# Kernel optimization log

Measured on AMD Instinct MI355X. Metric: run time of the kernel, lower is better.

## Reference

```python
import jax, jax.numpy as jnp
import numpy as np

B, N, D, H, K, T = 32, 4096, 256, 4, 8, 3
D_H = D // H
SCALE = D_H ** -0.5
EPS = 1e-8
LN_EPS = 1e-5


def _ln(x, g, b):
    m = x.mean(-1, keepdims=True)
    v = ((x - m) ** 2).mean(-1, keepdims=True)
    return (x - m) / jnp.sqrt(v + LN_EPS) * g + b


def _split(t):  # [b, n, D] -> [b, H, n, d_h]
    b, n, _ = t.shape
    return t.reshape(b, n, H, D_H).transpose(0, 2, 1, 3)


def _merge(t):  # [b, H, n, d_h] -> [b, n, D]
    b, h, n, d = t.shape
    return t.transpose(0, 2, 1, 3).reshape(b, n, h * d)


def setup_inputs() -> dict:
    key = jax.random.key(0)
    ks = jax.random.split(key, 12)
    init = lambda k, shape: (jax.random.normal(k, shape, jnp.float32) * 0.02)
    mu = jnp.tile(jnp.linspace(-1.0, 1.0, K)[:, None], (1, D))[None]  # [1,K,D]
    return {
        'x': jax.random.normal(ks[0], (B, N, D), jnp.float32),
        'mu': mu,
        'w_q': init(ks[1], (D, D)),
        'w_k': init(ks[2], (D, D)),
        'w_v': init(ks[3], (D, D)),
        'w_comb': init(ks[4], (D, D)),
        'g_in': jnp.ones(D), 'b_in': jnp.zeros(D),
        'g_slot': jnp.ones(D), 'b_slot': jnp.zeros(D),
        'g_mlp': jnp.ones(D), 'b_mlp': jnp.zeros(D),
        'w_ih': init(ks[5], (3 * D, D)),
        'w_hh': init(ks[6], (3 * D, D)),
        'b_ih': jnp.zeros(3 * D),
        'b_hh': jnp.zeros(3 * D),
        'w1': init(ks[7], (D, D)), 'b1': jnp.zeros(D),
        'w2': init(ks[8], (D, D)), 'b2': jnp.zeros(D),
    }


def reference(x, mu, w_q, w_k, w_v, w_comb, g_in, b_in, g_slot, b_slot,
              g_mlp, b_mlp, w_ih, w_hh, b_ih, b_hh, w1, b1, w2, b2):
    b = x.shape[0]
    x_norm = _ln(x, g_in, b_in)
    k_feat = _split(x_norm @ w_k.T)  # [b,H,N,d_h]
    v_feat = _split(x_norm @ w_v.T)

    def gru(u, h):  # torch GRUCell semantics
        gi = u @ w_ih.T + b_ih
        gh = h @ w_hh.T + b_hh
        ir, iz, i_n = jnp.split(gi, 3, axis=-1)
        hr, hz, h_n = jnp.split(gh, 3, axis=-1)
        r = jax.nn.sigmoid(ir + hr)
        z = jax.nn.sigmoid(iz + hz)
        n = jnp.tanh(i_n + r * h_n)
        return (1.0 - z) * n + z * h

    def step(slots, _):
        q = _split(_ln(slots, g_slot, b_slot) @ w_q.T)  # [b,H,K,d_h]
        dots = jnp.einsum('bhkd,bhnd->bhkn', q, k_feat) * SCALE
        attn = jax.nn.softmax(dots, axis=-2)  # softmax over slots
        attn = attn / (attn.sum(axis=-1, keepdims=True) + EPS)  # renorm over inputs
        updates = _merge(jnp.einsum('bhkn,bhnd->bhkd', attn, v_feat)) @ w_comb.T
        new = gru(updates.reshape(-1, D), slots.reshape(-1, D)).reshape(slots.shape)
        hid = jnp.maximum(_ln(new, g_mlp, b_mlp) @ w1.T + b1, 0.0)
        new = new + (hid @ w2.T + b2)
        return new, None

    slots0 = jnp.broadcast_to(mu, (b, K, D))  # eval mode: slots = mu
    slots, _ = jax.lax.scan(step, slots0, None, length=T)
    return slots
```

## Files before the change

kernel.cpp:

```cpp
#include <hip/hip_runtime.h>

#define BB 32
#define NN 4096
#define DD 256
#define HH 4
#define KK 8
#define DH 64

typedef unsigned short u16;
typedef unsigned int u32;
typedef __attribute__((ext_vector_type(8))) short short8;
typedef __attribute__((ext_vector_type(4))) float f32x4;

__device__ __forceinline__ float b2f(u16 u){ return __uint_as_float(((u32)u)<<16); }
__device__ __forceinline__ u16 f2b(float f){
  u32 u = __float_as_uint(f);
  u32 r = (u + 0x7fffu + ((u>>16)&1u)) >> 16;
  return (u16)r;
}

__global__ __launch_bounds__(256) void prep_kernel(
    const float* __restrict__ mu, const float* __restrict__ w_q,
    const float* __restrict__ w_k, const float* __restrict__ w_v,
    const float* __restrict__ w_comb, const float* __restrict__ w_ih,
    const float* __restrict__ w_hh, const float* __restrict__ w1,
    const float* __restrict__ w2,
    u16* __restrict__ wkv, u16* __restrict__ wq_b, u16* __restrict__ wcomb_b,
    u16* __restrict__ wih_b, u16* __restrict__ whh_b, u16* __restrict__ w1_b,
    u16* __restrict__ w2_b, float* __restrict__ slots)
{
  int i = blockIdx.x*256 + threadIdx.x;
  if (i < 131072) {
    int c = i>>8, d = i&255;
    float v = (c<256) ? w_k[c*256+d] : w_v[(c-256)*256+d];
    int off = (c<<9) + ((2*d) ^ ((c&15)<<4));
    wkv[off>>1] = f2b(v);
    return;
  }
  i -= 131072;
  if (i < 65536){ wq_b[i] = f2b(w_q[i]); return; } i -= 65536;
  if (i < 65536){ wcomb_b[i] = f2b(w_comb[i]); return; } i -= 65536;
  if (i < 196608){ wih_b[i] = f2b(w_ih[i]); return; } i -= 196608;
  if (i < 196608){ whh_b[i] = f2b(w_hh[i]); return; } i -= 196608;
  if (i < 65536){ w1_b[i] = f2b(w1[i]); return; } i -= 65536;
  if (i < 65536){ w2_b[i] = f2b(w2[i]); return; } i -= 65536;
  if (i < 65536){ slots[i] = mu[i & 2047]; return; }
}

__global__ __launch_bounds__(512,4) void kv_proj_kernel(
    const float* __restrict__ x, const float* __restrict__ g_in,
    const float* __restrict__ b_in, const u16* __restrict__ wkv,
    u16* __restrict__ Kmat, u16* __restrict__ Vmat)
{
  __shared__ __align__(16) u16 Atile[64*256];
  __shared__ __align__(16) u16 Btile[64*256];
  __shared__ __align__(16) u16 Cbuf[64*64];
  const int tid = threadIdx.x;
  const int w = tid>>6, l = tid&63;
  const long row0 = (long)blockIdx.x * 64;

  short8 breg[4];
  #pragma unroll
  for (int i=0;i<4;++i)
    breg[i] = *(const short8*)((const char*)wkv + (i*512 + tid)*16);

  const f32x4 gv = *(const f32x4*)(g_in + l*4);
  const f32x4 bv = *(const f32x4*)(b_in + l*4);

  #pragma unroll
  for (int rr=0; rr<8; ++rr) {
    const int r = w*8 + rr;
    const f32x4 xv = *(const f32x4*)(x + (row0+r)*DD + l*4);
    float s = xv.x+xv.y+xv.z+xv.w;
    float s2 = xv.x*xv.x+xv.y*xv.y+xv.z*xv.z+xv.w*xv.w;
    #pragma unroll
    for (int m=1;m<64;m<<=1){ s += __shfl_xor(s,m); s2 += __shfl_xor(s2,m); }
    const float mean = s * (1.f/256.f);
    const float rstd = rsqrtf(s2*(1.f/256.f) - mean*mean + 1e-5f);
    const u32 p0 = (u32)f2b((xv.x-mean)*rstd*gv.x + bv.x) | ((u32)f2b((xv.y-mean)*rstd*gv.y + bv.y)<<16);
    const u32 p1 = (u32)f2b((xv.z-mean)*rstd*gv.z + bv.z) | ((u32)f2b((xv.w-mean)*rstd*gv.w + bv.w)<<16);
    const unsigned long long pp = (unsigned long long)p0 | ((unsigned long long)p1<<32);
    *(unsigned long long*)((char*)Atile + r*512 + ((l*8) ^ ((r&15)<<4))) = pp;
  }
  #pragma unroll
  for (int i=0;i<4;++i)
    *(short8*)((char*)Btile + (i*512+tid)*16) = breg[i];
  __syncthreads();

  const int wm = w>>2, wn = w&3;
  const int lr = l&15;
  const int lk = (l>>4)*8;

  short8 afr0[8], afr1[8];
  #pragma unroll
  for (int ks=0; ks<8; ++ks) {
    const int k2 = (ks*32 + lk)*2;
    const int r0r = wm*32 + lr;
    const int r1r = wm*32 + 16 + lr;
    afr0[ks] = *(const short8*)((const char*)Atile + r0r*512 + (k2 ^ ((r0r&15)<<4)));
    afr1[ks] = *(const short8*)((const char*)Atile + r1r*512 + (k2 ^ ((r1r&15)<<4)));
  }
  #pragma unroll
  for (int ks=0; ks<8; ++ks) {
    asm volatile("" : "+v"(afr0[ks]));
    asm volatile("" : "+v"(afr1[ks]));
  }

  for (int ct=0; ct<8; ++ct) {
    short8 nreg[4];
    if (ct < 7) {
      #pragma unroll
      for (int i=0;i<4;++i)
        nreg[i] = *(const short8*)((const char*)wkv + (ct+1)*32768 + (i*512 + tid)*16);
    }

    f32x4 acc0 = (f32x4)0.f, acc1 = (f32x4)0.f;
    #pragma unroll
    for (int ks=0; ks<8; ++ks) {
      const int k2 = (ks*32 + lk)*2;
      const int c = wn*16 + lr;
      const short8 bfv = *(const short8*)((const char*)Btile + c*512 + (k2 ^ ((c&15)<<4)));
      acc0 = __builtin_amdgcn_mfma_f32_16x16x32_bf16(afr0[ks], bfv, acc0, 0,0,0);
      acc1 = __builtin_amdgcn_mfma_f32_16x16x32_bf16(afr1[ks], bfv, acc1, 0,0,0);
    }

    {
      const int c = wn*16 + lr;
      #pragma unroll
      for (int reg=0; reg<4; ++reg) {
        const int r0r = wm*32 + (l>>4)*4 + reg;
        const int r1r = r0r + 16;
        *(u16*)((char*)Cbuf + r0r*128 + ((2*c) ^ ((r0r&7)<<4))) = f2b(acc0[reg]);
        *(u16*)((char*)Cbuf + r1r*128 + ((2*c) ^ ((r1r&7)<<4))) = f2b(acc1[reg]);
      }
    }
    __syncthreads();

    if (ct < 7) {
      #pragma unroll
      for (int i=0;i<4;++i)
        *(short8*)((char*)Btile + (i*512+tid)*16) = nreg[i];
    }
    {
      const int r = tid>>3, cg = tid&7;
      const short8 vv = *(const short8*)((char*)Cbuf + r*128 + ((cg*16) ^ ((r&7)<<4)));
      u16* dst = (ct<4) ? Kmat : Vmat;
      *(short8*)(dst + (row0+r)*DD + (ct&3)*64 + cg*8) = vv;
    }
    __syncthreads();
  }
}

__global__ __launch_bounds__(256) void slot_q_kernel(
    const float* __restrict__ slots, const float* __restrict__ g_slot,
    const float* __restrict__ b_slot, const u16* __restrict__ wq_b,
    float* __restrict__ qmat)
{
  __shared__ float xn[256];
  __shared__ float red[8];
  const int r = blockIdx.x, t = threadIdx.x;
  const int w = t>>6, l = t&63;
  const float xv = slots[r*256 + t];
  float s = xv, s2 = xv*xv;
  #pragma unroll
  for (int m=1;m<64;m<<=1){ s += __shfl_xor(s,m); s2 += __shfl_xor(s2,m); }
  if (l==0){ red[w*2]=s; red[w*2+1]=s2; }
  __syncthreads();
  s = red[0]+red[2]+red[4]+red[6];
  s2 = red[1]+red[3]+red[5]+red[7];
  const float mean = s*(1.f/256.f);
  const float rstd = rsqrtf(s2*(1.f/256.f)-mean*mean + 1e-5f);
  xn[t] = (xv-mean)*rstd*g_slot[t] + b_slot[t];
  __syncthreads();
  const u16* wr = wq_b + t*256;
  float a0=0,a1=0,a2=0,a3=0;
  for (int d=0; d<256; d+=8) {
    const short8 wv = *(const short8*)(wr + d);
    a0 = fmaf(b2f((u16)wv[0]), xn[d+0], a0);
    a1 = fmaf(b2f((u16)wv[1]), xn[d+1], a1);
    a2 = fmaf(b2f((u16)wv[2]), xn[d+2], a2);
    a3 = fmaf(b2f((u16)wv[3]), xn[d+3], a3);
    a0 = fmaf(b2f((u16)wv[4]), xn[d+4], a0);
    a1 = fmaf(b2f((u16)wv[5]), xn[d+5], a1);
    a2 = fmaf(b2f((u16)wv[6]), xn[d+6], a2);
    a3 = fmaf(b2f((u16)wv[7]), xn[d+7], a3);
  }
  qmat[r*256 + t] = ((a0+a1)+(a2+a3));
}

__global__ __launch_bounds__(256) void attn_kernel(
    const u16* __restrict__ Kmat, const u16* __restrict__ Vmat,
    const float* __restrict__ qmat, float* __restrict__ U_part,
    float* __restrict__ S_part)
{
  __shared__ float U_lds[4][8][64];
  __shared__ float S_lds[4][8];
  const int bid = blockIdx.x;
  const int part = bid & 3, h = (bid>>2)&3, b = bid>>4;
  const int t = threadIdx.x, w = t>>6, l = t&63;
  const int ds = l&7, ng = l>>3;

  float qreg[8][8];
  #pragma unroll
  for (int k=0;k<8;++k) {
    const f32x4 qa = *(const f32x4*)(qmat + (b*8+k)*256 + h*64 + ds*8);
    const f32x4 qb = *(const f32x4*)(qmat + (b*8+k)*256 + h*64 + ds*8 + 4);
    qreg[k][0]=qa.x; qreg[k][1]=qa.y; qreg[k][2]=qa.z; qreg[k][3]=qa.w;
    qreg[k][4]=qb.x; qreg[k][5]=qb.y; qreg[k][6]=qb.z; qreg[k][7]=qb.w;
  }

  float accU[8][8];
  float sacc[8];
  #pragma unroll
  for (int k=0;k<8;++k){ sacc[k]=0.f;
    #pragma unroll
    for (int j=0;j<8;++j) accU[k][j]=0.f; }

  const long base = ((long)b*NN)*DD + h*64;
  const u16* Kp = Kmat + base + (long)(part*1024 + w*8 + ng)*DD + ds*8;
  const u16* Vp = Vmat + base + (long)(part*1024 + w*8 + ng)*DD + ds*8;

  short8 kc = *(const short8*)Kp;
  short8 vc = *(const short8*)Vp;
  for (int pass=0; pass<32; ++pass) {
    short8 kn, vn;
    if (pass < 31) {
      kn = *(const short8*)(Kp + (pass+1)*32*DD);
      vn = *(const short8*)(Vp + (pass+1)*32*DD);
    }
    float kd[8];
    #pragma unroll
    for (int j=0;j<8;++j) kd[j] = b2f((u16)kc[j]);
    float dots[8];
    #pragma unroll
    for (int k=0;k<8;++k) {
      float d0 = qreg[k][0]*kd[0] + qreg[k][1]*kd[1] + qreg[k][2]*kd[2] + qreg[k][3]*kd[3]
               + qreg[k][4]*kd[4] + qreg[k][5]*kd[5] + qreg[k][6]*kd[6] + qreg[k][7]*kd[7];
      d0 += __shfl_xor(d0,1); d0 += __shfl_xor(d0,2); d0 += __shfl_xor(d0,4);
      dots[k] = d0 * 0.125f;
    }
    float mx = dots[0];
    #pragma unroll
    for (int k=1;k<8;++k) mx = fmaxf(mx, dots[k]);
    float e[8]; float se = 0.f;
    #pragma unroll
    for (int k=0;k<8;++k){ e[k] = __expf(dots[k]-mx); se += e[k]; }
    const float inv = 1.f/se;
    float vd[8];
    #pragma unroll
    for (int j=0;j<8;++j) vd[j] = b2f((u16)vc[j]);
    #pragma unroll
    for (int k=0;k<8;++k) {
      const float p = e[k]*inv;
      sacc[k] += p;
      #pragma unroll
      for (int j=0;j<8;++j) accU[k][j] = fmaf(p, vd[j], accU[k][j]);
    }
    kc = kn; vc = vn;
  }
  #pragma unroll
  for (int k=0;k<8;++k){
    #pragma unroll
    for (int j=0;j<8;++j){
      float v = accU[k][j];
      v += __shfl_xor(v,8); v += __shfl_xor(v,16); v += __shfl_xor(v,32);
      accU[k][j]=v;
    }
    float sv = sacc[k];
    sv += __shfl_xor(sv,8); sv += __shfl_xor(sv,16); sv += __shfl_xor(sv,32);
    sacc[k]=sv;
  }
  if (l<8){
    #pragma unroll
    for (int k=0;k<8;++k)
      #pragma unroll
      for (int j=0;j<8;++j) U_lds[w][k][l*8+j] = accU[k][j];
  }
  if (l==0){
    #pragma unroll
    for (int k=0;k<8;++k) S_lds[w][k]=sacc[k];
  }
  __syncthreads();
  for (int i=t;i<512;i+=256){
    const int k=i>>6, d=i&63;
    U_part[(((long)part*32 + b)*4 + h)*512 + k*64 + d] =
      U_lds[0][k][d]+U_lds[1][k][d]+U_lds[2][k][d]+U_lds[3][k][d];
  }
  if (t<8){
    S_part[((part*32 + b)*4 + h)*8 + t] = S_lds[0][t]+S_lds[1][t]+S_lds[2][t]+S_lds[3][t];
  }
}

__global__ __launch_bounds__(256) void slot_update_kernel(
    const float* __restrict__ U_part, const float* __restrict__ S_part,
    float* __restrict__ slots,
    const u16* __restrict__ wcomb_b, const u16* __restrict__ wih_b,
    const u16* __restrict__ whh_b, const u16* __restrict__ w1_b,
    const u16* __restrict__ w2_b,
    const float* __restrict__ b_ih, const float* __restrict__ b_hh,
    const float* __restrict__ g_mlp, const float* __restrict__ b_mlp,
    const float* __restrict__ b1v, const float* __restrict__ b2v,
    const u16* __restrict__ wq_b, const float* __restrict__ g_slot,
    const float* __restrict__ b_slot, float* __restrict__ qmat,
    float* __restrict__ out_final, const int write_out, const int compute_q)
{
  __shared__ float uL[2][256];
  __shared__ float hL[2][256];
  __shared__ float cL[2][256];
  __shared__ float xL[2][256];
  __shared__ float red[16];
  const int blk = blockIdx.x, t = threadIdx.x;
  const int w = t>>6, l = t&63;
  const int r0 = blk*2;

  #pragma unroll
  for (int rr=0;rr<2;++rr) hL[rr][t] = slots[(r0+rr)*256 + t];

  #pragma unroll
  for (int rr=0;rr<2;++rr) {
    const int r = r0+rr, b = r>>3, k = r&7;
    const int h = t>>6, d = t&63;
    float ssum = 0.f, usum = 0.f;
    #pragma unroll
    for (int p=0;p<4;++p) {
      ssum += S_part[((p*32 + b)*4 + h)*8 + k];
      usum += U_part[(((long)p*32 + b)*4 + h)*512 + k*64 + d];
    }
    uL[rr][t] = usum / (ssum + 1e-8f);
  }
  __syncthreads();

  {
    float c00=0,c01=0,c10=0,c11=0;
    const u16* wr = wcomb_b + t*256;
    for (int d0=0; d0<256; d0+=8) {
      const short8 wv = *(const short8*)(wr + d0);
      float wf[8];
      #pragma unroll
      for (int j=0;j<8;++j) wf[j]=b2f((u16)wv[j]);
      #pragma unroll
      for (int j=0;j<8;j+=2) {
        c00 = fmaf(wf[j],   uL[0][d0+j],   c00);
        c01 = fmaf(wf[j+1], uL[0][d0+j+1], c01);
        c10 = fmaf(wf[j],   uL[1][d0+j],   c10);
        c11 = fmaf(wf[j+1], uL[1][d0+j+1], c11);
      }
    }
    cL[0][t]=c00+c01; cL[1][t]=c10+c11;
  }
  __syncthreads();

  float gi[3][2], gh[3][2];
  #pragma unroll
  for (int g=0; g<3; ++g){ gi[g][0]=0; gi[g][1]=0; gh[g][0]=0; gh[g][1]=0; }
  for (int d0=0; d0<256; d0+=8) {
    float u0[8],u1[8],h0[8],h1[8];
    #pragma unroll
    for (int j=0;j<8;j+=4) {
      *(f32x4*)&u0[j] = *(const f32x4*)&cL[0][d0+j];
      *(f32x4*)&u1[j] = *(const f32x4*)&cL[1][d0+j];
      *(f32x4*)&h0[j] = *(const f32x4*)&hL[0][d0+j];
      *(f32x4*)&h1[j] = *(const f32x4*)&hL[1][d0+j];
    }
    #pragma unroll
    for (int g=0; g<3; ++g) {
      const short8 wi = *(const short8*)(wih_b + (g*256+t)*256 + d0);
      const short8 wh = *(const short8*)(whh_b + (g*256+t)*256 + d0);
      #pragma unroll
      for (int j=0;j<8;++j) {
        const float a = b2f((u16)wi[j]);
        const float bw = b2f((u16)wh[j]);
        gi[g][0] = fmaf(a, u0[j], gi[g][0]);
        gi[g][1] = fmaf(a, u1[j], gi[g][1]);
        gh[g][0] = fmaf(bw, h0[j], gh[g][0]);
        gh[g][1] = fmaf(bw, h1[j], gh[g][1]);
      }
    }
  }
  float newv[2];
  #pragma unroll
  for (int rr=0;rr<2;++rr) {
    const float ir = gi[0][rr] + b_ih[t];
    const float iz = gi[1][rr] + b_ih[256+t];
    const float inn= gi[2][rr] + b_ih[512+t];
    const float hr = gh[0][rr] + b_hh[t];
    const float hz = gh[1][rr] + b_hh[256+t];
    const float hn = gh[2][rr] + b_hh[512+t];
    const float rg = 1.f/(1.f + __expf(-(ir+hr)));
    const float zg = 1.f/(1.f + __expf(-(iz+hz)));
    float targ = inn + rg*hn;
    targ = fminf(fmaxf(targ, -15.f), 15.f);
    const float ex = __expf(2.f*targ);
    const float ng = (ex-1.f)/(ex+1.f);
    newv[rr] = (1.f-zg)*ng + zg*hL[rr][t];
  }

  float s0=newv[0], q0=newv[0]*newv[0], s1=newv[1], q1=newv[1]*newv[1];
  #pragma unroll
  for (int m=1;m<64;m<<=1){
    s0+=__shfl_xor(s0,m); q0+=__shfl_xor(q0,m);
    s1+=__shfl_xor(s1,m); q1+=__shfl_xor(q1,m);
  }
  if (l==0){ red[w*4]=s0; red[w*4+1]=q0; red[w*4+2]=s1; red[w*4+3]=q1; }
  __syncthreads();
  s0 = red[0]+red[4]+red[8]+red[12];
  q0 = red[1]+red[5]+red[9]+red[13];
  s1 = red[2]+red[6]+red[10]+red[14];
  q1 = red[3]+red[7]+red[11]+red[15];
  {
    const float m0 = s0*(1.f/256.f), m1 = s1*(1.f/256.f);
    const float r0v = rsqrtf(q0*(1.f/256.f)-m0*m0 + 1e-5f);
    const float r1v = rsqrtf(q1*(1.f/256.f)-m1*m1 + 1e-5f);
    xL[0][t] = (newv[0]-m0)*r0v*g_mlp[t] + b_mlp[t];
    xL[1][t] = (newv[1]-m1)*r1v*g_mlp[t] + b_mlp[t];
  }
  __syncthreads();

  {
    float c00=0,c01=0,c10=0,c11=0;
    const u16* wr = w1_b + t*256;
    for (int d0=0; d0<256; d0+=8) {
      const short8 wv = *(const short8*)(wr + d0);
      float wf[8];
      #pragma unroll
      for (int j=0;j<8;++j) wf[j]=b2f((u16)wv[j]);
      #pragma unroll
      for (int j=0;j<8;j+=2) {
        c00 = fmaf(wf[j],   xL[0][d0+j],   c00);
        c01 = fmaf(wf[j+1], xL[0][d0+j+1], c01);
        c10 = fmaf(wf[j],   xL[1][d0+j],   c10);
        c11 = fmaf(wf[j+1], xL[1][d0+j+1], c11);
      }
    }
    uL[0][t] = fmaxf(c00+c01 + b1v[t], 0.f);
    uL[1][t] = fmaxf(c10+c11 + b1v[t], 0.f);
  }
  __syncthreads();

  float o0, o1;
  {
    float c00=0,c01=0,c10=0,c11=0;
    const u16* wr = w2_b + t*256;
    for (int d0=0; d0<256; d0+=8) {
      const short8 wv = *(const short8*)(wr + d0);
      float wf[8];
      #pragma unroll
      for (int j=0;j<8;++j) wf[j]=b2f((u16)wv[j]);
      #pragma unroll
      for (int j=0;j<8;j+=2) {
        c00 = fmaf(wf[j],   uL[0][d0+j],   c00);
        c01 = fmaf(wf[j+1], uL[0][d0+j+1], c01);
        c10 = fmaf(wf[j],   uL[1][d0+j],   c10);
        c11 = fmaf(wf[j+1], uL[1][d0+j+1], c11);
      }
    }
    o0 = newv[0] + c00+c01 + b2v[t];
    o1 = newv[1] + c10+c11 + b2v[t];
    slots[(r0+0)*256 + t] = o0;
    slots[(r0+1)*256 + t] = o1;
    if (write_out){
      out_final[(r0+0)*256 + t] = o0;
      out_final[(r0+1)*256 + t] = o1;
    }
  }

  if (compute_q) {
    __syncthreads();
    float t0=o0, p0=o0*o0, t1=o1, p1=o1*o1;
    #pragma unroll
    for (int m=1;m<64;m<<=1){
      t0+=__shfl_xor(t0,m); p0+=__shfl_xor(p0,m);
      t1+=__shfl_xor(t1,m); p1+=__shfl_xor(p1,m);
    }
    if (l==0){ red[w*4]=t0; red[w*4+1]=p0; red[w*4+2]=t1; red[w*4+3]=p1; }
    __syncthreads();
    t0 = red[0]+red[4]+red[8]+red[12];
    p0 = red[1]+red[5]+red[9]+red[13];
    t1 = red[2]+red[6]+red[10]+red[14];
    p1 = red[3]+red[7]+red[11]+red[15];
    const float m0 = t0*(1.f/256.f), m1 = t1*(1.f/256.f);
    const float r0v = rsqrtf(p0*(1.f/256.f)-m0*m0 + 1e-5f);
    const float r1v = rsqrtf(p1*(1.f/256.f)-m1*m1 + 1e-5f);
    cL[0][t] = (o0-m0)*r0v*g_slot[t] + b_slot[t];
    cL[1][t] = (o1-m1)*r1v*g_slot[t] + b_slot[t];
    __syncthreads();
    float c00=0,c01=0,c10=0,c11=0;
    const u16* wr = wq_b + t*256;
    for (int d0=0; d0<256; d0+=8) {
      const short8 wv = *(const short8*)(wr + d0);
      float wf[8];
      #pragma unroll
      for (int j=0;j<8;++j) wf[j]=b2f((u16)wv[j]);
      #pragma unroll
      for (int j=0;j<8;j+=2) {
        c00 = fmaf(wf[j],   cL[0][d0+j],   c00);
        c01 = fmaf(wf[j+1], cL[0][d0+j+1], c01);
        c10 = fmaf(wf[j],   cL[1][d0+j],   c10);
        c11 = fmaf(wf[j+1], cL[1][d0+j+1], c11);
      }
    }
    qmat[(r0+0)*256 + t] = c00+c01;
    qmat[(r0+1)*256 + t] = c10+c11;
  }
}

extern "C" void kernel_launch(void* const* d_in, const int* in_sizes, int n_in,
                              void* d_out, int out_size, void* d_ws, size_t ws_size,
                              hipStream_t stream)
{
  (void)in_sizes; (void)n_in; (void)out_size; (void)ws_size;
  const float* x      = (const float*)d_in[0];
  const float* mu     = (const float*)d_in[1];
  const float* w_q    = (const float*)d_in[2];
  const float* w_k    = (const float*)d_in[3];
  const float* w_v    = (const float*)d_in[4];
  const float* w_comb = (const float*)d_in[5];
  const float* g_in   = (const float*)d_in[6];
  const float* b_in   = (const float*)d_in[7];
  const float* g_slot = (const float*)d_in[8];
  const float* b_slot = (const float*)d_in[9];
  const float* g_mlp  = (const float*)d_in[10];
  const float* b_mlp  = (const float*)d_in[11];
  const float* w_ih   = (const float*)d_in[12];
  const float* w_hh   = (const float*)d_in[13];
  const float* b_ih   = (const float*)d_in[14];
  const float* b_hh   = (const float*)d_in[15];
  const float* w1     = (const float*)d_in[16];
  const float* b1     = (const float*)d_in[17];
  const float* w2     = (const float*)d_in[18];
  const float* b2     = (const float*)d_in[19];

  char* ws = (char*)d_ws;
  u16* Kmat    = (u16*)(ws + 0);
  u16* Vmat    = (u16*)(ws + 67108864);
  u16* wkv     = (u16*)(ws + 134217728);
  u16* wq_b    = (u16*)(ws + 134479872);
  u16* wcomb_b = (u16*)(ws + 134610944);
  u16* wih_b   = (u16*)(ws + 134742016);
  u16* whh_b   = (u16*)(ws + 135135232);
  u16* w1_b    = (u16*)(ws + 135528448);
  u16* w2_b    = (u16*)(ws + 135659520);
  float* slots = (float*)(ws + 135790592);
  float* qmat  = (float*)(ws + 136052736);
  float* U_part= (float*)(ws + 136314880);
  float* S_part= (float*)(ws + 137363456);

  hipLaunchKernelGGL(prep_kernel, dim3(3328), dim3(256), 0, stream,
                     mu, w_q, w_k, w_v, w_comb, w_ih, w_hh, w1, w2,
                     wkv, wq_b, wcomb_b, wih_b, whh_b, w1_b, w2_b, slots);
  hipLaunchKernelGGL(kv_proj_kernel, dim3(2048), dim3(512), 0, stream,
                     x, g_in, b_in, wkv, Kmat, Vmat);
  hipLaunchKernelGGL(slot_q_kernel, dim3(256), dim3(256), 0, stream,
                     slots, g_slot, b_slot, wq_b, qmat);
  float* outp = (float*)d_out;
  for (int it=0; it<3; ++it) {
    hipLaunchKernelGGL(attn_kernel, dim3(512), dim3(256), 0, stream,
                       Kmat, Vmat, qmat, U_part, S_part);
    hipLaunchKernelGGL(slot_update_kernel, dim3(128), dim3(256), 0, stream,
                       U_part, S_part, slots, wcomb_b, wih_b, whh_b, w1_b, w2_b,
                       b_ih, b_hh, g_mlp, b_mlp, b1, b2,
                       wq_b, g_slot, b_slot, qmat,
                       outp, (it==2)?1:0, (it<2)?1:0);
  }
}
```

Before: 350.2 us.

## Fuse attention and slot-update iterations into one cooperative persistent kernel

Replaces six alternating attention and slot-update launches with a single cooperative kernel that loops over the three iterations and uses grid-wide syncs between phases. Blocks stride over the attention work units and the slot-update rows. The aim is to remove kernel launch and drain gaps between the short dependent stages. In exchange it adds grid.sync overhead and a launch_bounds occupancy hint of 2 blocks per CU, which may cost registers in the heavy attention loop. The grid size also depends on the occupancy query, and with 256 blocks each block would do two attention units.

```diff
diff --git a/kernel.cpp b/kernel.cpp
--- a/kernel.cpp
+++ b/kernel.cpp
@@ -1,4 +1,5 @@
 #include <hip/hip_runtime.h>
+#include <hip/hip_cooperative_groups.h>
 
 #define BB 32
 #define NN 4096
@@ -188,111 +189,9 @@
   qmat[r*256 + t] = ((a0+a1)+(a2+a3));
 }
 
-__global__ __launch_bounds__(256) void attn_kernel(
+__global__ __launch_bounds__(256,2) void mega_kernel(
     const u16* __restrict__ Kmat, const u16* __restrict__ Vmat,
-    const float* __restrict__ qmat, float* __restrict__ U_part,
-    float* __restrict__ S_part)
-{
-  __shared__ float U_lds[4][8][64];
-  __shared__ float S_lds[4][8];
-  const int bid = blockIdx.x;
-  const int part = bid & 3, h = (bid>>2)&3, b = bid>>4;
-  const int t = threadIdx.x, w = t>>6, l = t&63;
-  const int ds = l&7, ng = l>>3;
-
-  float qreg[8][8];
-  #pragma unroll
-  for (int k=0;k<8;++k) {
-    const f32x4 qa = *(const f32x4*)(qmat + (b*8+k)*256 + h*64 + ds*8);
-    const f32x4 qb = *(const f32x4*)(qmat + (b*8+k)*256 + h*64 + ds*8 + 4);
-    qreg[k][0]=qa.x; qreg[k][1]=qa.y; qreg[k][2]=qa.z; qreg[k][3]=qa.w;
-    qreg[k][4]=qb.x; qreg[k][5]=qb.y; qreg[k][6]=qb.z; qreg[k][7]=qb.w;
-  }
-
-  float accU[8][8];
-  float sacc[8];
-  #pragma unroll
-  for (int k=0;k<8;++k){ sacc[k]=0.f;
-    #pragma unroll
-    for (int j=0;j<8;++j) accU[k][j]=0.f; }
-
-  const long base = ((long)b*NN)*DD + h*64;
-  const u16* Kp = Kmat + base + (long)(part*1024 + w*8 + ng)*DD + ds*8;
-  const u16* Vp = Vmat + base + (long)(part*1024 + w*8 + ng)*DD + ds*8;
-
-  short8 kc = *(const short8*)Kp;
-  short8 vc = *(const short8*)Vp;
-  for (int pass=0; pass<32; ++pass) {
-    short8 kn, vn;
-    if (pass < 31) {
-      kn = *(const short8*)(Kp + (pass+1)*32*DD);
-      vn = *(const short8*)(Vp + (pass+1)*32*DD);
-    }
-    float kd[8];
-    #pragma unroll
-    for (int j=0;j<8;++j) kd[j] = b2f((u16)kc[j]);
-    float dots[8];
-    #pragma unroll
-    for (int k=0;k<8;++k) {
-      float d0 = qreg[k][0]*kd[0] + qreg[k][1]*kd[1] + qreg[k][2]*kd[2] + qreg[k][3]*kd[3]
-               + qreg[k][4]*kd[4] + qreg[k][5]*kd[5] + qreg[k][6]*kd[6] + qreg[k][7]*kd[7];
-      d0 += __shfl_xor(d0,1); d0 += __shfl_xor(d0,2); d0 += __shfl_xor(d0,4);
-      dots[k] = d0 * 0.125f;
-    }
-    float mx = dots[0];
-    #pragma unroll
-    for (int k=1;k<8;++k) mx = fmaxf(mx, dots[k]);
-    float e[8]; float se = 0.f;
-    #pragma unroll
-    for (int k=0;k<8;++k){ e[k] = __expf(dots[k]-mx); se += e[k]; }
-    const float inv = 1.f/se;
-    float vd[8];
-    #pragma unroll
-    for (int j=0;j<8;++j) vd[j] = b2f((u16)vc[j]);
-    #pragma unroll
-    for (int k=0;k<8;++k) {
-      const float p = e[k]*inv;
-      sacc[k] += p;
-      #pragma unroll
-      for (int j=0;j<8;++j) accU[k][j] = fmaf(p, vd[j], accU[k][j]);
-    }
-    kc = kn; vc = vn;
-  }
-  #pragma unroll
-  for (int k=0;k<8;++k){
-    #pragma unroll
-    for (int j=0;j<8;++j){
-      float v = accU[k][j];
-      v += __shfl_xor(v,8); v += __shfl_xor(v,16); v += __shfl_xor(v,32);
-      accU[k][j]=v;
-    }
-    float sv = sacc[k];
-    sv += __shfl_xor(sv,8); sv += __shfl_xor(sv,16); sv += __shfl_xor(sv,32);
-    sacc[k]=sv;
-  }
-  if (l<8){
-    #pragma unroll
-    for (int k=0;k<8;++k)
-      #pragma unroll
-      for (int j=0;j<8;++j) U_lds[w][k][l*8+j] = accU[k][j];
-  }
-  if (l==0){
-    #pragma unroll
-    for (int k=0;k<8;++k) S_lds[w][k]=sacc[k];
-  }
-  __syncthreads();
-  for (int i=t;i<512;i+=256){
-    const int k=i>>6, d=i&63;
-    U_part[(((long)part*32 + b)*4 + h)*512 + k*64 + d] =
-      U_lds[0][k][d]+U_lds[1][k][d]+U_lds[2][k][d]+U_lds[3][k][d];
-  }
-  if (t<8){
-    S_part[((part*32 + b)*4 + h)*8 + t] = S_lds[0][t]+S_lds[1][t]+S_lds[2][t]+S_lds[3][t];
-  }
-}
-
-__global__ __launch_bounds__(256) void slot_update_kernel(
-    const float* __restrict__ U_part, const float* __restrict__ S_part,
+    float* __restrict__ qmat, float* __restrict__ U_part, float* __restrict__ S_part,
     float* __restrict__ slots,
     const u16* __restrict__ wcomb_b, const u16* __restrict__ wih_b,
     const u16* __restrict__ whh_b, const u16* __restrict__ w1_b,
@@ -301,206 +200,317 @@
     const float* __restrict__ g_mlp, const float* __restrict__ b_mlp,
     const float* __restrict__ b1v, const float* __restrict__ b2v,
     const u16* __restrict__ wq_b, const float* __restrict__ g_slot,
-    const float* __restrict__ b_slot, float* __restrict__ qmat,
-    float* __restrict__ out_final, const int write_out, const int compute_q)
+    const float* __restrict__ b_slot, float* __restrict__ out_final)
 {
+  cooperative_groups::grid_group grid = cooperative_groups::this_grid();
+  __shared__ float U_lds[4][8][64];
+  __shared__ float S_lds[4][8];
   __shared__ float uL[2][256];
   __shared__ float hL[2][256];
   __shared__ float cL[2][256];
   __shared__ float xL[2][256];
   __shared__ float red[16];
-  const int blk = blockIdx.x, t = threadIdx.x;
-  const int w = t>>6, l = t&63;
-  const int r0 = blk*2;
-
-  #pragma unroll
-  for (int rr=0;rr<2;++rr) hL[rr][t] = slots[(r0+rr)*256 + t];
-
-  #pragma unroll
-  for (int rr=0;rr<2;++rr) {
-    const int r = r0+rr, b = r>>3, k = r&7;
-    const int h = t>>6, d = t&63;
-    float ssum = 0.f, usum = 0.f;
-    #pragma unroll
-    for (int p=0;p<4;++p) {
-      ssum += S_part[((p*32 + b)*4 + h)*8 + k];
-      usum += U_part[(((long)p*32 + b)*4 + h)*512 + k*64 + d];
-    }
-    uL[rr][t] = usum / (ssum + 1e-8f);
-  }
-  __syncthreads();
-
-  {
-    float c00=0,c01=0,c10=0,c11=0;
-    const u16* wr = wcomb_b + t*256;
-    for (int d0=0; d0<256; d0+=8) {
-      const short8 wv = *(const short8*)(wr + d0);
-      float wf[8];
-      #pragma unroll
-      for (int j=0;j<8;++j) wf[j]=b2f((u16)wv[j]);
-      #pragma unroll
-      for (int j=0;j<8;j+=2) {
-        c00 = fmaf(wf[j],   uL[0][d0+j],   c00);
-        c01 = fmaf(wf[j+1], uL[0][d0+j+1], c01);
-        c10 = fmaf(wf[j],   uL[1][d0+j],   c10);
-        c11 = fmaf(wf[j+1], uL[1][d0+j+1], c11);
-      }
-    }
-    cL[0][t]=c00+c01; cL[1][t]=c10+c11;
-  }
-  __syncthreads();
-
-  float gi[3][2], gh[3][2];
-  #pragma unroll
-  for (int g=0; g<3; ++g){ gi[g][0]=0; gi[g][1]=0; gh[g][0]=0; gh[g][1]=0; }
-  for (int d0=0; d0<256; d0+=8) {
-    float u0[8],u1[8],h0[8],h1[8];
-    #pragma unroll
-    for (int j=0;j<8;j+=4) {
-      *(f32x4*)&u0[j] = *(const f32x4*)&cL[0][d0+j];
-      *(f32x4*)&u1[j] = *(const f32x4*)&cL[1][d0+j];
-      *(f32x4*)&h0[j] = *(const f32x4*)&hL[0][d0+j];
-      *(f32x4*)&h1[j] = *(const f32x4*)&hL[1][d0+j];
-    }
-    #pragma unroll
-    for (int g=0; g<3; ++g) {
-      const short8 wi = *(const short8*)(wih_b + (g*256+t)*256 + d0);
-      const short8 wh = *(const short8*)(whh_b + (g*256+t)*256 + d0);
-      #pragma unroll
-      for (int j=0;j<8;++j) {
-        const float a = b2f((u16)wi[j]);
-        const float bw = b2f((u16)wh[j]);
-        gi[g][0] = fmaf(a, u0[j], gi[g][0]);
-        gi[g][1] = fmaf(a, u1[j], gi[g][1]);
-        gh[g][0] = fmaf(bw, h0[j], gh[g][0]);
-        gh[g][1] = fmaf(bw, h1[j], gh[g][1]);
-      }
-    }
-  }
-  float newv[2];
-  #pragma unroll
-  for (int rr=0;rr<2;++rr) {
-    const float ir = gi[0][rr] + b_ih[t];
-    const float iz = gi[1][rr] + b_ih[256+t];
-    const float inn= gi[2][rr] + b_ih[512+t];
-    const float hr = gh[0][rr] + b_hh[t];
-    const float hz = gh[1][rr] + b_hh[256+t];
-    const float hn = gh[2][rr] + b_hh[512+t];
-    const float rg = 1.f/(1.f + __expf(-(ir+hr)));
-    const float zg = 1.f/(1.f + __expf(-(iz+hz)));
-    float targ = inn + rg*hn;
-    targ = fminf(fmaxf(targ, -15.f), 15.f);
-    const float ex = __expf(2.f*targ);
-    const float ng = (ex-1.f)/(ex+1.f);
-    newv[rr] = (1.f-zg)*ng + zg*hL[rr][t];
-  }
-
-  float s0=newv[0], q0=newv[0]*newv[0], s1=newv[1], q1=newv[1]*newv[1];
-  #pragma unroll
-  for (int m=1;m<64;m<<=1){
-    s0+=__shfl_xor(s0,m); q0+=__shfl_xor(q0,m);
-    s1+=__shfl_xor(s1,m); q1+=__shfl_xor(q1,m);
-  }
-  if (l==0){ red[w*4]=s0; red[w*4+1]=q0; red[w*4+2]=s1; red[w*4+3]=q1; }
-  __syncthreads();
-  s0 = red[0]+red[4]+red[8]+red[12];
-  q0 = red[1]+red[5]+red[9]+red[13];
-  s1 = red[2]+red[6]+red[10]+red[14];
-  q1 = red[3]+red[7]+red[11]+red[15];
-  {
-    const float m0 = s0*(1.f/256.f), m1 = s1*(1.f/256.f);
-    const float r0v = rsqrtf(q0*(1.f/256.f)-m0*m0 + 1e-5f);
-    const float r1v = rsqrtf(q1*(1.f/256.f)-m1*m1 + 1e-5f);
-    xL[0][t] = (newv[0]-m0)*r0v*g_mlp[t] + b_mlp[t];
-    xL[1][t] = (newv[1]-m1)*r1v*g_mlp[t] + b_mlp[t];
-  }
-  __syncthreads();
-
-  {
-    float c00=0,c01=0,c10=0,c11=0;
-    const u16* wr = w1_b + t*256;
-    for (int d0=0; d0<256; d0+=8) {
-      const short8 wv = *(const short8*)(wr + d0);
-      float wf[8];
-      #pragma unroll
-      for (int j=0;j<8;++j) wf[j]=b2f((u16)wv[j]);
-      #pragma unroll
-      for (int j=0;j<8;j+=2) {
-        c00 = fmaf(wf[j],   xL[0][d0+j],   c00);
-        c01 = fmaf(wf[j+1], xL[0][d0+j+1], c01);
-        c10 = fmaf(wf[j],   xL[1][d0+j],   c10);
-        c11 = fmaf(wf[j+1], xL[1][d0+j+1], c11);
-      }
-    }
-    uL[0][t] = fmaxf(c00+c01 + b1v[t], 0.f);
-    uL[1][t] = fmaxf(c10+c11 + b1v[t], 0.f);
-  }
-  __syncthreads();
-
-  float o0, o1;
-  {
-    float c00=0,c01=0,c10=0,c11=0;
-    const u16* wr = w2_b + t*256;
-    for (int d0=0; d0<256; d0+=8) {
-      const short8 wv = *(const short8*)(wr + d0);
-      float wf[8];
-      #pragma unroll
-      for (int j=0;j<8;++j) wf[j]=b2f((u16)wv[j]);
-      #pragma unroll
-      for (int j=0;j<8;j+=2) {
-        c00 = fmaf(wf[j],   uL[0][d0+j],   c00);
-        c01 = fmaf(wf[j+1], uL[0][d0+j+1], c01);
-        c10 = fmaf(wf[j],   uL[1][d0+j],   c10);
-        c11 = fmaf(wf[j+1], uL[1][d0+j+1], c11);
-      }
-    }
-    o0 = newv[0] + c00+c01 + b2v[t];
-    o1 = newv[1] + c10+c11 + b2v[t];
-    slots[(r0+0)*256 + t] = o0;
-    slots[(r0+1)*256 + t] = o1;
-    if (write_out){
-      out_final[(r0+0)*256 + t] = o0;
-      out_final[(r0+1)*256 + t] = o1;
-    }
-  }
-
-  if (compute_q) {
-    __syncthreads();
-    float t0=o0, p0=o0*o0, t1=o1, p1=o1*o1;
-    #pragma unroll
-    for (int m=1;m<64;m<<=1){
-      t0+=__shfl_xor(t0,m); p0+=__shfl_xor(p0,m);
-      t1+=__shfl_xor(t1,m); p1+=__shfl_xor(p1,m);
-    }
-    if (l==0){ red[w*4]=t0; red[w*4+1]=p0; red[w*4+2]=t1; red[w*4+3]=p1; }
-    __syncthreads();
-    t0 = red[0]+red[4]+red[8]+red[12];
-    p0 = red[1]+red[5]+red[9]+red[13];
-    t1 = red[2]+red[6]+red[10]+red[14];
-    p1 = red[3]+red[7]+red[11]+red[15];
-    const float m0 = t0*(1.f/256.f), m1 = t1*(1.f/256.f);
-    const float r0v = rsqrtf(p0*(1.f/256.f)-m0*m0 + 1e-5f);
-    const float r1v = rsqrtf(p1*(1.f/256.f)-m1*m1 + 1e-5f);
-    cL[0][t] = (o0-m0)*r0v*g_slot[t] + b_slot[t];
-    cL[1][t] = (o1-m1)*r1v*g_slot[t] + b_slot[t];
-    __syncthreads();
-    float c00=0,c01=0,c10=0,c11=0;
-    const u16* wr = wq_b + t*256;
-    for (int d0=0; d0<256; d0+=8) {
-      const short8 wv = *(const short8*)(wr + d0);
-      float wf[8];
-      #pragma unroll
-      for (int j=0;j<8;++j) wf[j]=b2f((u16)wv[j]);
-      #pragma unroll
-      for (int j=0;j<8;j+=2) {
-        c00 = fmaf(wf[j],   cL[0][d0+j],   c00);
-        c01 = fmaf(wf[j+1], cL[0][d0+j+1], c01);
-        c10 = fmaf(wf[j],   cL[1][d0+j],   c10);
-        c11 = fmaf(wf[j+1], cL[1][d0+j+1], c11);
-      }
-    }
-    qmat[(r0+0)*256 + t] = c00+c01;
-    qmat[(r0+1)*256 + t] = c10+c11;
+
+  const int G = gridDim.x;
+  const int t = threadIdx.x, w = t>>6, l = t&63;
+
+  for (int it=0; it<3; ++it) {
+    for (int u = blockIdx.x; u < 512; u += G) {
+      const int part = u & 3, h = (u>>2)&3, b = u>>4;
+      const int ds = l&7, ng = l>>3;
+
+      float qreg[8][8];
+      #pragma unroll
+      for (int k=0;k<8;++k) {
+        const f32x4 qa = *(const f32x4*)(qmat + (b*8+k)*256 + h*64 + ds*8);
+        const f32x4 qb = *(const f32x4*)(qmat + (b*8+k)*256 + h*64 + ds*8 + 4);
+        qreg[k][0]=qa.x; qreg[k][1]=qa.y; qreg[k][2]=qa.z; qreg[k][3]=qa.w;
+        qreg[k][4]=qb.x; qreg[k][5]=qb.y; qreg[k][6]=qb.z; qreg[k][7]=qb.w;
+      }
+
+      float accU[8][8];
+      float sacc[8];
+      #pragma unroll
+      for (int k=0;k<8;++k){ sacc[k]=0.f;
+        #pragma unroll
+        for (int j=0;j<8;++j) accU[k][j]=0.f; }
+
+      const long base = ((long)b*NN)*DD + h*64;
+      const u16* Kp = Kmat + base + (long)(part*1024 + w*8 + ng)*DD + ds*8;
+      const u16* Vp = Vmat + base + (long)(part*1024 + w*8 + ng)*DD + ds*8;
+
+      short8 kc = *(const short8*)Kp;
+      short8 vc = *(const short8*)Vp;
+      for (int pass=0; pass<32; ++pass) {
+        short8 kn = kc, vn = vc;
+        if (pass < 31) {
+          kn = *(const short8*)(Kp + (pass+1)*32*DD);
+          vn = *(const short8*)(Vp + (pass+1)*32*DD);
+        }
+        float kd[8];
+        #pragma unroll
+        for (int j=0;j<8;++j) kd[j] = b2f((u16)kc[j]);
+        float dots[8];
+        #pragma unroll
+        for (int k=0;k<8;++k) {
+          float d0 = qreg[k][0]*kd[0] + qreg[k][1]*kd[1] + qreg[k][2]*kd[2] + qreg[k][3]*kd[3]
+                   + qreg[k][4]*kd[4] + qreg[k][5]*kd[5] + qreg[k][6]*kd[6] + qreg[k][7]*kd[7];
+          d0 += __shfl_xor(d0,1); d0 += __shfl_xor(d0,2); d0 += __shfl_xor(d0,4);
+          dots[k] = d0 * 0.125f;
+        }
+        float mx = dots[0];
+        #pragma unroll
+        for (int k=1;k<8;++k) mx = fmaxf(mx, dots[k]);
+        float e[8]; float se = 0.f;
+        #pragma unroll
+        for (int k=0;k<8;++k){ e[k] = __expf(dots[k]-mx); se += e[k]; }
+        const float inv = 1.f/se;
+        float vd[8];
+        #pragma unroll
+        for (int j=0;j<8;++j) vd[j] = b2f((u16)vc[j]);
+        #pragma unroll
+        for (int k=0;k<8;++k) {
+          const float p = e[k]*inv;
+          sacc[k] += p;
+          #pragma unroll
+          for (int j=0;j<8;++j) accU[k][j] = fmaf(p, vd[j], accU[k][j]);
+        }
+        kc = kn; vc = vn;
+      }
+      #pragma unroll
+      for (int k=0;k<8;++k){
+        #pragma unroll
+        for (int j=0;j<8;++j){
+          float v = accU[k][j];
+          v += __shfl_xor(v,8); v += __shfl_xor(v,16); v += __shfl_xor(v,32);
+          accU[k][j]=v;
+        }
+        float sv = sacc[k];
+        sv += __shfl_xor(sv,8); sv += __shfl_xor(sv,16); sv += __shfl_xor(sv,32);
+        sacc[k]=sv;
+      }
+      __syncthreads();
+      if (l<8){
+        #pragma unroll
+        for (int k=0;k<8;++k)
+          #pragma unroll
+          for (int j=0;j<8;++j) U_lds[w][k][l*8+j] = accU[k][j];
+      }
+      if (l==0){
+        #pragma unroll
+        for (int k=0;k<8;++k) S_lds[w][k]=sacc[k];
+      }
+      __syncthreads();
+      for (int i=t;i<512;i+=256){
+        const int k=i>>6, d=i&63;
+        U_part[(((long)part*32 + b)*4 + h)*512 + k*64 + d] =
+          U_lds[0][k][d]+U_lds[1][k][d]+U_lds[2][k][d]+U_lds[3][k][d];
+      }
+      if (t<8){
+        S_part[((part*32 + b)*4 + h)*8 + t] = S_lds[0][t]+S_lds[1][t]+S_lds[2][t]+S_lds[3][t];
+      }
+    }
+
+    grid.sync();
+
+    for (int u = blockIdx.x; u < 128; u += G) {
+      const int write_out = (it==2), compute_q = (it<2);
+      const int r0 = u*2;
+
+      __syncthreads();
+
+      #pragma unroll
+      for (int rr=0;rr<2;++rr) hL[rr][t] = slots[(r0+rr)*256 + t];
+
+      #pragma unroll
+      for (int rr=0;rr<2;++rr) {
+        const int r = r0+rr, b = r>>3, k = r&7;
+        const int h = t>>6, d = t&63;
+        float ssum = 0.f, usum = 0.f;
+        #pragma unroll
+        for (int p=0;p<4;++p) {
+          ssum += S_part[((p*32 + b)*4 + h)*8 + k];
+          usum += U_part[(((long)p*32 + b)*4 + h)*512 + k*64 + d];
+        }
+        uL[rr][t] = usum / (ssum + 1e-8f);
+      }
+      __syncthreads();
+
+      {
+        float c00=0,c01=0,c10=0,c11=0;
+        const u16* wr = wcomb_b + t*256;
+        for (int d0=0; d0<256; d0+=8) {
+          const short8 wv = *(const short8*)(wr + d0);
+          float wf[8];
+          #pragma unroll
+          for (int j=0;j<8;++j) wf[j]=b2f((u16)wv[j]);
+          #pragma unroll
+          for (int j=0;j<8;j+=2) {
+            c00 = fmaf(wf[j],   uL[0][d0+j],   c00);
+            c01 = fmaf(wf[j+1], uL[0][d0+j+1], c01);
+            c10 = fmaf(wf[j],   uL[1][d0+j],   c10);
+            c11 = fmaf(wf[j+1], uL[1][d0+j+1], c11);
+          }
+        }
+        cL[0][t]=c00+c01; cL[1][t]=c10+c11;
+      }
+      __syncthreads();
+
+      float gi[3][2], gh[3][2];
+      #pragma unroll
+      for (int g=0; g<3; ++g){ gi[g][0]=0; gi[g][1]=0; gh[g][0]=0; gh[g][1]=0; }
+      for (int d0=0; d0<256; d0+=8) {
+        float u0[8],u1[8],h0[8],h1[8];
+        #pragma unroll
+        for (int j=0;j<8;j+=4) {
+          *(f32x4*)&u0[j] = *(const f32x4*)&cL[0][d0+j];
+          *(f32x4*)&u1[j] = *(const f32x4*)&cL[1][d0+j];
+          *(f32x4*)&h0[j] = *(const f32x4*)&hL[0][d0+j];
+          *(f32x4*)&h1[j] = *(const f32x4*)&hL[1][d0+j];
+        }
+        #pragma unroll
+        for (int g=0; g<3; ++g) {
+          const short8 wi = *(const short8*)(wih_b + (g*256+t)*256 + d0);
+          const short8 wh = *(const short8*)(whh_b + (g*256+t)*256 + d0);
+          #pragma unroll
+          for (int j=0;j<8;++j) {
+            const float a = b2f((u16)wi[j]);
+            const float bw = b2f((u16)wh[j]);
+            gi[g][0] = fmaf(a, u0[j], gi[g][0]);
+            gi[g][1] = fmaf(a, u1[j], gi[g][1]);
+            gh[g][0] = fmaf(bw, h0[j], gh[g][0]);
+            gh[g][1] = fmaf(bw, h1[j], gh[g][1]);
+          }
+        }
+      }
+      float newv[2];
+      #pragma unroll
+      for (int rr=0;rr<2;++rr) {
+        const float ir = gi[0][rr] + b_ih[t];
+        const float iz = gi[1][rr] + b_ih[256+t];
+        const float inn= gi[2][rr] + b_ih[512+t];
+        const float hr = gh[0][rr] + b_hh[t];
+        const float hz = gh[1][rr] + b_hh[256+t];
+        const float hn = gh[2][rr] + b_hh[512+t];
+        const float rg = 1.f/(1.f + __expf(-(ir+hr)));
+        const float zg = 1.f/(1.f + __expf(-(iz+hz)));
+        float targ = inn + rg*hn;
+        targ = fminf(fmaxf(targ, -15.f), 15.f);
+        const float ex = __expf(2.f*targ);
+        const float ng = (ex-1.f)/(ex+1.f);
+        newv[rr] = (1.f-zg)*ng + zg*hL[rr][t];
+      }
+
+      float s0=newv[0], q0=newv[0]*newv[0], s1=newv[1], q1=newv[1]*newv[1];
+      #pragma unroll
+      for (int m=1;m<64;m<<=1){
+        s0+=__shfl_xor(s0,m); q0+=__shfl_xor(q0,m);
+        s1+=__shfl_xor(s1,m); q1+=__shfl_xor(q1,m);
+      }
+      if (l==0){ red[w*4]=s0; red[w*4+1]=q0; red[w*4+2]=s1; red[w*4+3]=q1; }
+      __syncthreads();
+      s0 = red[0]+red[4]+red[8]+red[12];
+      q0 = red[1]+red[5]+red[9]+red[13];
+      s1 = red[2]+red[6]+red[10]+red[14];
+      q1 = red[3]+red[7]+red[11]+red[15];
+      {
+        const float m0 = s0*(1.f/256.f), m1 = s1*(1.f/256.f);
+        const float r0v = rsqrtf(q0*(1.f/256.f)-m0*m0 + 1e-5f);
+        const float r1v = rsqrtf(q1*(1.f/256.f)-m1*m1 + 1e-5f);
+        xL[0][t] = (newv[0]-m0)*r0v*g_mlp[t] + b_mlp[t];
+        xL[1][t] = (newv[1]-m1)*r1v*g_mlp[t] + b_mlp[t];
+      }
+      __syncthreads();
+
+      {
+        float c00=0,c01=0,c10=0,c11=0;
+        const u16* wr = w1_b + t*256;
+        for (int d0=0; d0<256; d0+=8) {
+          const short8 wv = *(const short8*)(wr + d0);
+          float wf[8];
+          #pragma unroll
+          for (int j=0;j<8;++j) wf[j]=b2f((u16)wv[j]);
+          #pragma unroll
+          for (int j=0;j<8;j+=2) {
+            c00 = fmaf(wf[j],   xL[0][d0+j],   c00);
+            c01 = fmaf(wf[j+1], xL[0][d0+j+1], c01);
+            c10 = fmaf(wf[j],   xL[1][d0+j],   c10);
+            c11 = fmaf(wf[j+1], xL[1][d0+j+1], c11);
+          }
+        }
+        uL[0][t] = fmaxf(c00+c01 + b1v[t], 0.f);
+        uL[1][t] = fmaxf(c10+c11 + b1v[t], 0.f);
+      }
+      __syncthreads();
+
+      float o0, o1;
+      {
+        float c00=0,c01=0,c10=0,c11=0;
+        const u16* wr = w2_b + t*256;
+        for (int d0=0; d0<256; d0+=8) {
+          const short8 wv = *(const short8*)(wr + d0);
+          float wf[8];
+          #pragma unroll
+          for (int j=0;j<8;++j) wf[j]=b2f((u16)wv[j]);
+          #pragma unroll
+          for (int j=0;j<8;j+=2) {
+            c00 = fmaf(wf[j],   uL[0][d0+j],   c00);
+            c01 = fmaf(wf[j+1], uL[0][d0+j+1], c01);
+            c10 = fmaf(wf[j],   uL[1][d0+j],   c10);
+            c11 = fmaf(wf[j+1], uL[1][d0+j+1], c11);
+          }
+        }
+        o0 = newv[0] + c00+c01 + b2v[t];
+        o1 = newv[1] + c10+c11 + b2v[t];
+        slots[(r0+0)*256 + t] = o0;
+        slots[(r0+1)*256 + t] = o1;
+        if (write_out){
+          out_final[(r0+0)*256 + t] = o0;
+          out_final[(r0+1)*256 + t] = o1;
+        }
+      }
+
+      if (compute_q) {
+        __syncthreads();
+        float t0=o0, p0=o0*o0, t1=o1, p1=o1*o1;
+        #pragma unroll
+        for (int m=1;m<64;m<<=1){
+          t0+=__shfl_xor(t0,m); p0+=__shfl_xor(p0,m);
+          t1+=__shfl_xor(t1,m); p1+=__shfl_xor(p1,m);
+        }
+        if (l==0){ red[w*4]=t0; red[w*4+1]=p0; red[w*4+2]=t1; red[w*4+3]=p1; }
+        __syncthreads();
+        t0 = red[0]+red[4]+red[8]+red[12];
+        p0 = red[1]+red[5]+red[9]+red[13];
+        t1 = red[2]+red[6]+red[10]+red[14];
+        p1 = red[3]+red[7]+red[11]+red[15];
+        const float m0 = t0*(1.f/256.f), m1 = t1*(1.f/256.f);
+        const float r0v = rsqrtf(p0*(1.f/256.f)-m0*m0 + 1e-5f);
+        const float r1v = rsqrtf(p1*(1.f/256.f)-m1*m1 + 1e-5f);
+        cL[0][t] = (o0-m0)*r0v*g_slot[t] + b_slot[t];
+        cL[1][t] = (o1-m1)*r1v*g_slot[t] + b_slot[t];
+        __syncthreads();
+        float c00=0,c01=0,c10=0,c11=0;
+        const u16* wr = wq_b + t*256;
+        for (int d0=0; d0<256; d0+=8) {
+          const short8 wv = *(const short8*)(wr + d0);
+          float wf[8];
+          #pragma unroll
+          for (int j=0;j<8;++j) wf[j]=b2f((u16)wv[j]);
+          #pragma unroll
+          for (int j=0;j<8;j+=2) {
+            c00 = fmaf(wf[j],   cL[0][d0+j],   c00);
+            c01 = fmaf(wf[j+1], cL[0][d0+j+1], c01);
+            c10 = fmaf(wf[j],   cL[1][d0+j],   c10);
+            c11 = fmaf(wf[j+1], cL[1][d0+j+1], c11);
+          }
+        }
+        qmat[(r0+0)*256 + t] = c00+c01;
+        qmat[(r0+1)*256 + t] = c10+c11;
+      }
+    }
+
+    grid.sync();
   }
 }
 
@@ -552,14 +562,19 @@
                      x, g_in, b_in, wkv, Kmat, Vmat);
   hipLaunchKernelGGL(slot_q_kernel, dim3(256), dim3(256), 0, stream,
                      slots, g_slot, b_slot, wq_b, qmat);
+
+  int nb = 0;
+  (void)hipOccupancyMaxActiveBlocksPerMultiprocessor(&nb, mega_kernel, 256, 0);
+  int gridN = 256;
+  if (nb >= 2) gridN = 512;
+
   float* outp = (float*)d_out;
-  for (int it=0; it<3; ++it) {
-    hipLaunchKernelGGL(attn_kernel, dim3(512), dim3(256), 0, stream,
-                       Kmat, Vmat, qmat, U_part, S_part);
-    hipLaunchKernelGGL(slot_update_kernel, dim3(128), dim3(256), 0, stream,
-                       U_part, S_part, slots, wcomb_b, wih_b, whh_b, w1_b, w2_b,
-                       b_ih, b_hh, g_mlp, b_mlp, b1, b2,
-                       wq_b, g_slot, b_slot, qmat,
-                       outp, (it==2)?1:0, (it<2)?1:0);
-  }
+  void* args[] = {
+    (void*)&Kmat, (void*)&Vmat, (void*)&qmat, (void*)&U_part, (void*)&S_part,
+    (void*)&slots, (void*)&wcomb_b, (void*)&wih_b, (void*)&whh_b, (void*)&w1_b,
+    (void*)&w2_b, (void*)&b_ih, (void*)&b_hh, (void*)&g_mlp, (void*)&b_mlp,
+    (void*)&b1, (void*)&b2, (void*)&wq_b, (void*)&g_slot, (void*)&b_slot,
+    (void*)&outp
+  };
+  hipLaunchCooperativeKernel(mega_kernel, dim3(gridN), dim3(256), args, 0, stream);
 }
```

New measurement: 867.0 us. +147.6%, slower.

## Split attention into per-row softmax phase staged in LDS, then PV accumulation

Applied to the files above, without the earlier changes.

The attention kernel now runs in two phases. First, each thread computes a full 64-wide dot product for one key row against Q held in LDS, then the slot softmax, and writes the probabilities to a 32KB LDS buffer. Second, the threads accumulate P·V from that buffer. This removes the per-row cross-lane shuffle reductions and the softmax duplicated across 8 lanes. In exchange it adds large per-thread register arrays, more LDS use, and an extra barrier, and it serialises the K and V streaming. Launch bounds also request four blocks per SM.

```diff
diff --git a/kernel.cpp b/kernel.cpp
--- a/kernel.cpp
+++ b/kernel.cpp
@@ -188,27 +188,65 @@
   qmat[r*256 + t] = ((a0+a1)+(a2+a3));
 }
 
-__global__ __launch_bounds__(256) void attn_kernel(
+__global__ __launch_bounds__(256,4) void attn_kernel(
     const u16* __restrict__ Kmat, const u16* __restrict__ Vmat,
     const float* __restrict__ qmat, float* __restrict__ U_part,
     float* __restrict__ S_part)
 {
+  __shared__ float Q_lds[8][64];
+  __shared__ float P_lds[8][1024];
   __shared__ float U_lds[4][8][64];
   __shared__ float S_lds[4][8];
   const int bid = blockIdx.x;
   const int part = bid & 3, h = (bid>>2)&3, b = bid>>4;
   const int t = threadIdx.x, w = t>>6, l = t&63;
+
+  for (int i=t; i<512; i+=256) {
+    const int k = i>>6, d = i&63;
+    Q_lds[k][d] = qmat[(b*8+k)*256 + h*64 + d];
+  }
+  __syncthreads();
+
+  const long base = ((long)b*NN)*DD + h*64;
+
+  for (int pass=0; pass<4; ++pass) {
+    const int rl = pass*256 + w*64 + l;
+    const u16* Kp = Kmat + base + (long)(part*1024 + rl)*DD;
+    short8 kr[8];
+    #pragma unroll
+    for (int j=0;j<8;++j) kr[j] = *(const short8*)(Kp + j*8);
+    float kf[64];
+    #pragma unroll
+    for (int j=0;j<8;++j)
+      #pragma unroll
+      for (int e=0;e<8;++e) kf[j*8+e] = b2f((u16)kr[j][e]);
+    float dots[8];
+    #pragma unroll
+    for (int k=0;k<8;++k) {
+      float a0=0,a1=0,a2=0,a3=0;
+      #pragma unroll
+      for (int d=0; d<64; d+=4) {
+        const f32x4 qv = *(const f32x4*)&Q_lds[k][d];
+        a0 = fmaf(kf[d+0], qv.x, a0);
+        a1 = fmaf(kf[d+1], qv.y, a1);
+        a2 = fmaf(kf[d+2], qv.z, a2);
+        a3 = fmaf(kf[d+3], qv.w, a3);
+      }
+      dots[k] = ((a0+a1)+(a2+a3)) * 0.125f;
+    }
+    float mx = dots[0];
+    #pragma unroll
+    for (int k=1;k<8;++k) mx = fmaxf(mx, dots[k]);
+    float e[8]; float se = 0.f;
+    #pragma unroll
+    for (int k=0;k<8;++k){ e[k] = __expf(dots[k]-mx); se += e[k]; }
+    const float inv = 1.f/se;
+    #pragma unroll
+    for (int k=0;k<8;++k) P_lds[k][rl] = e[k]*inv;
+  }
+  __syncthreads();
+
   const int ds = l&7, ng = l>>3;
-
-  float qreg[8][8];
-  #pragma unroll
-  for (int k=0;k<8;++k) {
-    const f32x4 qa = *(const f32x4*)(qmat + (b*8+k)*256 + h*64 + ds*8);
-    const f32x4 qb = *(const f32x4*)(qmat + (b*8+k)*256 + h*64 + ds*8 + 4);
-    qreg[k][0]=qa.x; qreg[k][1]=qa.y; qreg[k][2]=qa.z; qreg[k][3]=qa.w;
-    qreg[k][4]=qb.x; qreg[k][5]=qb.y; qreg[k][6]=qb.z; qreg[k][7]=qb.w;
-  }
-
   float accU[8][8];
   float sacc[8];
   #pragma unroll
@@ -216,47 +254,25 @@
     #pragma unroll
     for (int j=0;j<8;++j) accU[k][j]=0.f; }
 
-  const long base = ((long)b*NN)*DD + h*64;
-  const u16* Kp = Kmat + base + (long)(part*1024 + w*8 + ng)*DD + ds*8;
   const u16* Vp = Vmat + base + (long)(part*1024 + w*8 + ng)*DD + ds*8;
-
-  short8 kc = *(const short8*)Kp;
   short8 vc = *(const short8*)Vp;
   for (int pass=0; pass<32; ++pass) {
-    short8 kn, vn;
-    if (pass < 31) {
-      kn = *(const short8*)(Kp + (pass+1)*32*DD);
-      vn = *(const short8*)(Vp + (pass+1)*32*DD);
-    }
-    float kd[8];
-    #pragma unroll
-    for (int j=0;j<8;++j) kd[j] = b2f((u16)kc[j]);
-    float dots[8];
+    short8 vn = vc;
+    if (pass < 31) vn = *(const short8*)(Vp + (pass+1)*32*DD);
+    const int rl = pass*32 + w*8 + ng;
+    float p[8];
+    #pragma unroll
+    for (int k=0;k<8;++k) p[k] = P_lds[k][rl];
+    float vd[8];
+    #pragma unroll
+    for (int j=0;j<8;++j) vd[j] = b2f((u16)vc[j]);
     #pragma unroll
     for (int k=0;k<8;++k) {
-      float d0 = qreg[k][0]*kd[0] + qreg[k][1]*kd[1] + qreg[k][2]*kd[2] + qreg[k][3]*kd[3]
-               + qreg[k][4]*kd[4] + qreg[k][5]*kd[5] + qreg[k][6]*kd[6] + qreg[k][7]*kd[7];
-      d0 += __shfl_xor(d0,1); d0 += __shfl_xor(d0,2); d0 += __shfl_xor(d0,4);
-      dots[k] = d0 * 0.125f;
-    }
-    float mx = dots[0];
-    #pragma unroll
-    for (int k=1;k<8;++k) mx = fmaxf(mx, dots[k]);
-    float e[8]; float se = 0.f;
-    #pragma unroll
-    for (int k=0;k<8;++k){ e[k] = __expf(dots[k]-mx); se += e[k]; }
-    const float inv = 1.f/se;
-    float vd[8];
-    #pragma unroll
-    for (int j=0;j<8;++j) vd[j] = b2f((u16)vc[j]);
-    #pragma unroll
-    for (int k=0;k<8;++k) {
-      const float p = e[k]*inv;
-      sacc[k] += p;
-      #pragma unroll
-      for (int j=0;j<8;++j) accU[k][j] = fmaf(p, vd[j], accU[k][j]);
-    }
-    kc = kn; vc = vn;
+      sacc[k] += p[k];
+      #pragma unroll
+      for (int j=0;j<8;++j) accU[k][j] = fmaf(p[k], vd[j], accU[k][j]);
+    }
+    vc = vn;
   }
   #pragma unroll
   for (int k=0;k<8;++k){
```

After: 536.4 us. 1.53x slower.
